# Optimization experiments

Hardware: AMD Instinct MI355X
Metric: run time of the kernel (lower is better)

## Reference

```python
import jax, jax.numpy as jnp
from jax import lax
import numpy as np

B, N, M, V, K = 256, 16, 128, 512, 8
TAU = 1.0          # gumbel_temperature
PAD_IDX = 0        # y_vocab.token_to_idx('<PAD>')
NEG = -1e9


def setup_inputs() -> dict:
    key = jax.random.key(0)
    k1, k2, k3, k4, k5 = jax.random.split(key, 5)
    decodings = jax.random.uniform(k1, (B, N, M, V), dtype=jnp.float32)
    dec_logits = jax.random.normal(k2, (B, K, N + 1), dtype=jnp.float32)
    uniform_noise = jax.random.uniform(k3, (B, K, N + 1), dtype=jnp.float32,
                                       minval=1e-6, maxval=1.0 - 1e-6)
    target_types = jax.random.randint(k4, (B,), 0, 128)
    spans = jnp.clip(jax.random.randint(k5, (B,), 0, N + 1), 2, N)
    return {"decodings": decodings, "dec_logits": dec_logits,
            "uniform_noise": uniform_noise, "target_types": target_types,
            "spans": spans}


def _gumbel_softmax_hard(logits, u, tau):
    # straight-through hard gumbel-softmax, matching F.gumbel_softmax(hard=True)
    g = -jnp.log(-jnp.log(u))
    y_soft = jax.nn.softmax((logits + g) / tau, axis=-1)
    hard = jax.nn.one_hot(jnp.argmax(y_soft, axis=-1), logits.shape[-1],
                          dtype=y_soft.dtype)
    return hard + y_soft - lax.stop_gradient(y_soft)


def _build_dt_sample(dec_logits, uniform_noise, target_types, spans):
    # valid positions 0..spans[i] (i.e. spans[i]+1 entries); rest stay zero
    valid = (jnp.arange(N + 1)[None, None, :] <= spans[:, None, None])  # [B,1,N+1]
    masked = jnp.where(valid, dec_logits, NEG)
    logp = jax.nn.log_softmax(masked, axis=-1)          # log_softmax over span+1
    samp = _gumbel_softmax_hard(logp, uniform_noise, TAU)
    samp = samp * valid.astype(samp.dtype)              # zeros beyond span+1
    # start_template for target_type == 20: row 0 -> one-hot(1), rows 1..K-1 -> one-hot(0)
    start_idx = jnp.zeros((K,), dtype=jnp.int32).at[0].set(1)
    start_template = jax.nn.one_hot(start_idx, N + 1, dtype=samp.dtype)  # [K,N+1]
    is20 = (target_types == 20)[:, None, None]
    return jnp.where(is20, start_template[None], samp)   # [B,K,N+1]


def _apply_decoder_template(dt_sample, decodings):
    # choices[i] = [pad_onehot, flatten(decodings[i, n]) for n in range(N)]
    pad_flat = jax.nn.one_hot(PAD_IDX, M * V, dtype=decodings.dtype)      # [M*V]
    flat = decodings.reshape(B, N, M * V)
    choices = jnp.concatenate(
        [jnp.broadcast_to(pad_flat, (B, 1, M * V)), flat], axis=1)         # [B,N+1,M*V]
    # small contraction over N+1 -> memory bound
    outputs = jnp.einsum('bkn,bnf->bkf', dt_sample, choices)
    outputs = outputs.reshape(B, K, M, V)

    pos = jnp.arange(M)

    def place_one(outs_k):  # outs_k: [K, M, V] for one batch element
        def step(carry, out_t):
            result, idx = carry
            oidx = jnp.argmax(out_t, axis=-1)                              # [M]
            olen = jnp.max(jnp.where(oidx != 0, pos + 1, 0))
            olen = jnp.minimum(olen, M - idx)
            src = jnp.clip(pos - idx, 0, M - 1)
            mask = (pos >= idx) & (pos < idx + olen)
            result = jnp.where(mask[:, None], out_t[src], result)
            return (result, idx + olen), None
        (res, _), _ = lax.scan(step, (jnp.zeros((M, V), outs_k.dtype),
                                      jnp.int32(0)), outs_k)
        return res

    return jax.vmap(place_one)(outputs)                                    # [B,M,V]


def reference(decodings, dec_logits, uniform_noise, target_types, spans):
    dt_sample = _build_dt_sample(dec_logits, uniform_noise, target_types, spans)
    new_d = _apply_decoder_template(dt_sample, decodings)
    return new_d
```

## Files before the change

kernel.cpp:

```cpp
#include <hip/hip_runtime.h>
#include <hip/hip_bf16.h>
#include <math.h>

#define BB 256
#define NN 16
#define MM 128
#define VV 512
#define KK 8
#define NP1 17

__global__ __launch_bounds__(256) void phaseA(
        const float* __restrict__ decodings,
        const float* __restrict__ dec_logits,
        const float* __restrict__ noise,
        const int*   __restrict__ ttypes,
        const int*   __restrict__ spans,
        int* __restrict__ ws_idx,
        int* __restrict__ ws_olen)
{
    const int wave = (blockIdx.x * blockDim.x + threadIdx.x) >> 6;
    const int lane = threadIdx.x & 63;
    const int b = wave >> 3;
    const int k = wave & 7;

    int idx;
    if (ttypes[b] == 20) {
        idx = (k == 0) ? 1 : 0;
    } else {
        const int span = spans[b];
        float score = -INFINITY;
        int   bi    = 1000;
        if (lane < NP1) {
            const int base = (b * KK + k) * NP1 + lane;
            float logit = dec_logits[base];
            float u     = noise[base];
            float g     = -logf(-logf(u));
            float m     = (lane <= span) ? logit : -1e9f;
            score = m + g;
            bi    = lane;
        }
        for (int off = 32; off; off >>= 1) {
            float s2 = __shfl_down(score, off);
            int   b2 = __shfl_down(bi, off);
            if (s2 > score || (s2 == score && b2 < bi)) { score = s2; bi = b2; }
        }
        idx = __shfl(bi, 0);
    }

    int olen = 0;
    if (idx > 0) {
        const float* base = decodings + (((size_t)b * NN + (idx - 1)) * MM) * (size_t)VV;
        for (int m = MM - 1; m >= 0; --m) {
            const float4* row = (const float4*)(base + (size_t)m * VV);
            float4 a = row[lane];
            float4 c = row[64 + lane];
            float r0 = __shfl(a.x, 0);
            float mx = fmaxf(fmaxf(a.y, a.z), a.w);
            if (lane != 0) mx = fmaxf(mx, a.x);
            mx = fmaxf(mx, fmaxf(fmaxf(c.x, c.y), fmaxf(c.z, c.w)));
            for (int off = 32; off; off >>= 1) mx = fmaxf(mx, __shfl_xor(mx, off));
            if (mx > r0) { olen = m + 1; break; }
        }
    }

    if (lane == 0) {
        ws_idx[wave]  = idx;
        ws_olen[wave] = olen;
    }
}

__global__ __launch_bounds__(256) void phaseB(
        const float* __restrict__ decodings,
        const int*   __restrict__ ws_idx,
        const int*   __restrict__ ws_olen,
        float* __restrict__ out)
{
    const int b    = blockIdx.x >> 2;
    const int part = blockIdx.x & 3;
    const int tid  = threadIdx.x;

    __shared__ int s_src[32];
    if (tid < 32) {
        const int m_out = part * 32 + tid;
        int start = 0;
        int src   = -1;
        #pragma unroll
        for (int k = 0; k < KK; ++k) {
            int idx = ws_idx[b * KK + k];
            int ol  = ws_olen[b * KK + k];
            ol = min(ol, MM - start);
            if (m_out >= start && m_out < start + ol)
                src = (idx - 1) * MM + (m_out - start);
            start += ol;
        }
        s_src[tid] = src;
    }
    __syncthreads();

    const float4* dec4 = (const float4*)(decodings + (size_t)b * NN * MM * VV);
    float4*       out4 = (float4*)(out + ((size_t)b * MM + part * 32) * (size_t)VV);

    #pragma unroll
    for (int i = 0; i < 16; ++i) {
        int flat    = i * 256 + tid;
        int m_local = flat >> 7;
        int v4      = flat & 127;
        int s       = s_src[m_local];
        float4 val;
        if (s >= 0) val = dec4[(size_t)s * 128 + v4];
        else        val = make_float4(0.f, 0.f, 0.f, 0.f);
        out4[flat] = val;
    }
}

extern "C" void kernel_launch(void* const* d_in, const int* in_sizes, int n_in,
                              void* d_out, int out_size, void* d_ws, size_t ws_size,
                              hipStream_t stream) {
    const float* decodings  = (const float*)d_in[0];
    const float* dec_logits = (const float*)d_in[1];
    const float* noise      = (const float*)d_in[2];
    const int*   ttypes     = (const int*)d_in[3];
    const int*   spans      = (const int*)d_in[4];
    float* out = (float*)d_out;

    int* ws_idx  = (int*)d_ws;
    int* ws_olen = ws_idx + BB * KK;

    phaseA<<<(BB * KK) / 4, 256, 0, stream>>>(decodings, dec_logits, noise,
                                              ttypes, spans, ws_idx, ws_olen);
    phaseB<<<BB * 4, 256, 0, stream>>>(decodings, ws_idx, ws_olen, out);
}
```

Before: 30.76 us.

## Fuse index selection and row placement into one kernel

Merges the two kernels into a single launch. Each 512-thread block handles half of one batch element: its 8 waves compute the sampled index and output length per k into shared memory, then the block gathers 64 output rows. This removes a kernel launch and the global workspace round trip. In exchange, the phase-A work (gumbel argmax plus the backward scan over decoding rows) is now done twice per batch element, once by each of the two blocks.

```diff
diff --git a/kernel.cpp b/kernel.cpp
--- a/kernel.cpp
+++ b/kernel.cpp
@@ -9,19 +9,24 @@
 #define KK 8
 #define NP1 17
 
-__global__ __launch_bounds__(256) void phaseA(
+__global__ __launch_bounds__(512) void fused_place(
         const float* __restrict__ decodings,
         const float* __restrict__ dec_logits,
         const float* __restrict__ noise,
         const int*   __restrict__ ttypes,
         const int*   __restrict__ spans,
-        int* __restrict__ ws_idx,
-        int* __restrict__ ws_olen)
+        float* __restrict__ out)
 {
-    const int wave = (blockIdx.x * blockDim.x + threadIdx.x) >> 6;
-    const int lane = threadIdx.x & 63;
-    const int b = wave >> 3;
-    const int k = wave & 7;
+    const int b    = blockIdx.x >> 1;
+    const int part = blockIdx.x & 1;
+    const int tid  = threadIdx.x;
+    const int wave = tid >> 6;
+    const int lane = tid & 63;
+    const int k    = wave;
+
+    __shared__ int s_idx[KK];
+    __shared__ int s_olen[KK];
+    __shared__ int s_src[64];
 
     int idx;
     if (ttypes[b] == 20) {
@@ -64,33 +69,21 @@
     }
 
     if (lane == 0) {
-        ws_idx[wave]  = idx;
-        ws_olen[wave] = olen;
+        s_idx[k]  = idx;
+        s_olen[k] = olen;
     }
-}
+    __syncthreads();
 
-__global__ __launch_bounds__(256) void phaseB(
-        const float* __restrict__ decodings,
-        const int*   __restrict__ ws_idx,
-        const int*   __restrict__ ws_olen,
-        float* __restrict__ out)
-{
-    const int b    = blockIdx.x >> 2;
-    const int part = blockIdx.x & 3;
-    const int tid  = threadIdx.x;
-
-    __shared__ int s_src[32];
-    if (tid < 32) {
-        const int m_out = part * 32 + tid;
+    if (tid < 64) {
+        const int m_out = part * 64 + tid;
         int start = 0;
         int src   = -1;
         #pragma unroll
-        for (int k = 0; k < KK; ++k) {
-            int idx = ws_idx[b * KK + k];
-            int ol  = ws_olen[b * KK + k];
-            ol = min(ol, MM - start);
+        for (int kk = 0; kk < KK; ++kk) {
+            int id = s_idx[kk];
+            int ol = min(s_olen[kk], MM - start);
             if (m_out >= start && m_out < start + ol)
-                src = (idx - 1) * MM + (m_out - start);
+                src = (id - 1) * MM + (m_out - start);
             start += ol;
         }
         s_src[tid] = src;
@@ -98,11 +91,11 @@
     __syncthreads();
 
     const float4* dec4 = (const float4*)(decodings + (size_t)b * NN * MM * VV);
-    float4*       out4 = (float4*)(out + ((size_t)b * MM + part * 32) * (size_t)VV);
+    float4*       out4 = (float4*)(out + ((size_t)b * MM + part * 64) * (size_t)VV);
 
     #pragma unroll
     for (int i = 0; i < 16; ++i) {
-        int flat    = i * 256 + tid;
+        int flat    = i * 512 + tid;
         int m_local = flat >> 7;
         int v4      = flat & 127;
         int s       = s_src[m_local];
@@ -123,10 +116,6 @@
     const int*   spans      = (const int*)d_in[4];
     float* out = (float*)d_out;
 
-    int* ws_idx  = (int*)d_ws;
-    int* ws_olen = ws_idx + BB * KK;
-
-    phaseA<<<(BB * KK) / 4, 256, 0, stream>>>(decodings, dec_logits, noise,
-                                              ttypes, spans, ws_idx, ws_olen);
-    phaseB<<<BB * 4, 256, 0, stream>>>(decodings, ws_idx, ws_olen, out);
+    fused_place<<<BB * 2, 512, 0, stream>>>(decodings, dec_logits, noise,
+                                            ttypes, spans, out);
 }
```

Result: faster. 27.90 us (-9.3%).
